# Optimization experiments

Measured on AMD Instinct MI355X. Metric: run time of the kernel, lower is better.

The kernel has to match this reference:

```python
import jax, jax.numpy as jnp
import numpy as np
from jax import lax

L, B, S, D, V, NL = 64, 32, 64, 512, 32000, 2


def setup_inputs() -> dict:
    key = jax.random.key(0)
    ks = jax.random.split(key, 9)
    sd = 1.0 / np.sqrt(D)
    return {
        "rnn_input": jax.random.randint(ks[0], (L, B), 0, V),
        "last_hidden": jax.random.normal(ks[1], (NL, B, D), jnp.float32),
        "encoder_outputs": jax.random.normal(ks[2], (S, B, D), jnp.float32),
        "embed_table": jax.random.normal(ks[3], (V, D), jnp.float32) * sd,
        "sru_W": jax.random.normal(ks[4], (NL, D, 3 * D), jnp.float32) * sd,
        "sru_b": jax.random.normal(ks[5], (NL, 2 * D), jnp.float32) * 0.01,
        "attn_W": jax.random.normal(ks[6], (2 * D, D), jnp.float32) * sd,
        "out_W": jax.random.normal(ks[7], (D, V), jnp.float32) * sd,
        "out_b": jax.random.normal(ks[8], (V,), jnp.float32) * 0.01,
    }


def _sru_layer(x, c0, W, b):
    # x: [L,B,D] layer input, c0: [B,D], W: [D,3D], b: [2D]
    U = jnp.einsum('lbd,de->lbe', x, W)          # [L,B,3D]
    z, fp, rp = jnp.split(U, 3, axis=-1)          # candidate, forget, reset pre-acts
    bf, br = jnp.split(b, 2)
    f = jax.nn.sigmoid(fp + bf)
    r = jax.nn.sigmoid(rp + br)

    def step(c, inp):
        f_t, z_t = inp
        c = f_t * c + (1.0 - f_t) * z_t
        return c, c

    c_last, c_seq = lax.scan(step, c0, (f, z))    # c_seq: [L,B,D]
    h = r * jnp.tanh(c_seq) + (1.0 - r) * x       # highway (n_in == n_out)
    return h, c_last


def reference(rnn_input, last_hidden, encoder_outputs, embed_table, sru_W, sru_b, attn_W, out_W, out_b):
    x = embed_table[rnn_input]                    # [L,B,D]
    finals = []
    for l in range(NL):                           # small fixed layer loop
        x, c_last = _sru_layer(x, last_hidden[l], sru_W[l], sru_b[l])
        finals.append(c_last)
    hidden = jnp.stack(finals, axis=0)            # [NL,B,D]

    q = jnp.transpose(x, (1, 0, 2))               # [B,L,D]
    mem = jnp.transpose(encoder_outputs, (1, 0, 2))  # [B,S,D]
    scores = jnp.einsum('bld,bsd->bls', q, mem)   # dot attention
    align = jax.nn.softmax(scores, axis=-1)
    ctx = jnp.einsum('bls,bsd->bld', align, mem)
    attn_h = jnp.tanh(jnp.concatenate([ctx, q], axis=-1) @ attn_W)  # [B,L,D]
    output = attn_h @ out_W + out_b               # [B,L,V]
    return output, hidden
```

## Files before the change

kernel.cpp:

```cpp
#include <hip/hip_runtime.h>
#include <hip/hip_bf16.h>

#define L_ 64
#define B_ 32
#define S_ 64
#define D_ 512
#define V_ 32000
#define NL_ 2

typedef __attribute__((ext_vector_type(8))) short bf16x8;
typedef __attribute__((ext_vector_type(4))) float f32x4;

static __device__ __forceinline__ short f2bf(float f) {
  union { float f; unsigned u; } x; x.f = f;
  unsigned r = (x.u + 0x7FFFu + ((x.u >> 16) & 1u)) >> 16;
  return (short)r;
}

#define GLOAD_LDS16(g, l)                                                     \
  __builtin_amdgcn_global_load_lds(                                           \
      (const __attribute__((address_space(1))) void*)(g),                     \
      (__attribute__((address_space(3))) void*)(l), 16, 0, 0)

__global__ void prep_kernel(const float* __restrict__ sruW, const float* __restrict__ attnW,
                            const float* __restrict__ outW, const int* __restrict__ tok,
                            const float* __restrict__ tab,
                            short* __restrict__ WTs, short* __restrict__ WTa,
                            short* __restrict__ WTo,
                            float* __restrict__ xf, short* __restrict__ xb) {
  int bid = blockIdx.x;
  int tx = threadIdx.x, ty = threadIdx.y;
  __shared__ float tile[32][33];
  if (bid < 18048) {
    const float* in;
    short* out;
    int K, N, bx, by;
    if (bid < 1536) {
      int l = (bid >= 768) ? 1 : 0;
      int r = bid - l * 768;
      bx = r % 48; by = r / 48; K = 512; N = 1536;
      in = sruW + (size_t)l * 512 * 1536;
      out = WTs + (size_t)l * 1536 * 512;
    } else if (bid < 2048) {
      int r = bid - 1536;
      bx = r % 16; by = r / 16; K = 1024; N = 512;
      in = attnW; out = WTa;
    } else {
      int r = bid - 2048;
      bx = r % 1000; by = r / 1000; K = 512; N = 32000;
      in = outW; out = WTo;
    }
    int x = bx * 32 + tx;
    int y0 = by * 32;
    for (int j = ty; j < 32; j += 8) {
      int y = y0 + j;
      tile[j][tx] = (x < N && y < K) ? in[(size_t)y * N + x] : 0.f;
    }
    __syncthreads();
    int xo = y0 + tx;
    int yo0 = bx * 32;
    for (int j = ty; j < 32; j += 8) {
      int yo = yo0 + j;
      if (yo < N && xo < K) out[(size_t)yo * K + xo] = f2bf(tile[tx][j]);
    }
  } else {
    int i = (bid - 18048) * 256 + ty * 32 + tx;
    int d = i & (D_ - 1);
    int lb = i >> 9;
    float v = tab[(size_t)tok[lb] * D_ + d];
    xf[i] = v;
    xb[i] = f2bf(v);
  }
}

template <int BMt, int BNt, int WM, int WN, int MODE>
__global__ __launch_bounds__(256) void gemm_t(
    const short* __restrict__ A, const short* __restrict__ BT,
    void* __restrict__ Cptr, const float* __restrict__ bias,
    int M, int N, int K, int nbm) {
  constexpr int MI = BMt / WM / 16;
  constexpr int NI = BNt / WN / 16;
  constexpr int ACH = BMt / 8;
  constexpr int NCH = (BMt + BNt) / 8;
  constexpr int CPW = NCH / 4;

  const int nwg = gridDim.x;
  const int qc = nwg >> 3;
  const int bid = blockIdx.x;
  const int wg = (bid & 7) * qc + (bid >> 3);
  const int bm = wg % nbm;
  const int bn = wg / nbm;

  __shared__ __align__(16) short la[2][BMt * 64];
  __shared__ __align__(16) short lb[2][BNt * 64];
  const int tid = threadIdx.x;
  const int wave = tid >> 6, lane = tid & 63;
  const int wm = (wave / WN) * (BMt / WM);
  const int wn = (wave % WN) * (BNt / WN);

  f32x4 acc[MI][NI] = {};

  const int lrow = lane >> 3;
  const int lslot = lane & 7;
  const short* Abase = A + (size_t)(bm * BMt) * K;
  const short* Bbase = BT + (size_t)(bn * BNt) * K;

  auto stage = [&](int buf, int k0) {
#pragma unroll
    for (int c = 0; c < CPW; ++c) {
      int chunk = wave * CPW + c;
      if (chunk < ACH) {
        int row = chunk * 8 + lrow;
        int slot = lslot ^ (row & 7);
        GLOAD_LDS16(Abase + (size_t)row * K + k0 + slot * 8, &la[buf][chunk * 512]);
      } else {
        int bc = chunk - ACH;
        int row = bc * 8 + lrow;
        int slot = lslot ^ (row & 7);
        GLOAD_LDS16(Bbase + (size_t)row * K + k0 + slot * 8, &lb[buf][bc * 512]);
      }
    }
  };

  stage(0, 0);
  __syncthreads();

  const int nt = K / 64;
  int cur = 0;
  for (int t = 0; t < nt; ++t) {
    if (t + 1 < nt) stage(cur ^ 1, (t + 1) * 64);
#pragma unroll
    for (int kk = 0; kk < 2; ++kk) {
      bf16x8 af[MI], bfr[NI];
#pragma unroll
      for (int mi = 0; mi < MI; ++mi) {
        int row = wm + mi * 16 + (lane & 15);
        int slot = (kk * 4 + (lane >> 4)) ^ (row & 7);
        af[mi] = *(const bf16x8*)&la[cur][row * 64 + slot * 8];
      }
#pragma unroll
      for (int ni = 0; ni < NI; ++ni) {
        int row = wn + ni * 16 + (lane & 15);
        int slot = (kk * 4 + (lane >> 4)) ^ (row & 7);
        bfr[ni] = *(const bf16x8*)&lb[cur][row * 64 + slot * 8];
      }
#pragma unroll
      for (int mi = 0; mi < MI; ++mi)
#pragma unroll
        for (int ni = 0; ni < NI; ++ni)
          acc[mi][ni] = __builtin_amdgcn_mfma_f32_16x16x32_bf16(
              af[mi], bfr[ni], acc[mi][ni], 0, 0, 0);
    }
    __syncthreads();
    cur ^= 1;
  }

  const int cl = lane & 15;
  const int rl = (lane >> 4) * 4;
#pragma unroll
  for (int mi = 0; mi < MI; ++mi) {
#pragma unroll
    for (int ni = 0; ni < NI; ++ni) {
      int c = bn * BNt + wn + ni * 16 + cl;
      int r0 = bm * BMt + wm + mi * 16 + rl;
#pragma unroll
      for (int j = 0; j < 4; ++j) {
        int r = r0 + j;
        float v = acc[mi][ni][j];
        if (MODE == 0) {
          ((float*)Cptr)[(size_t)r * N + c] = v;
        } else if (MODE == 1) {
          ((short*)Cptr)[(size_t)r * N + c] = f2bf(tanhf(v));
        } else {
          int b = r & 31, l = r >> 5;
          ((float*)Cptr)[(size_t)(b * L_ + l) * N + c] = v + bias[c];
        }
      }
    }
  }
}

template <int MODE>
__global__ __launch_bounds__(256, 3) void gemm_s(
    const short* __restrict__ A, const short* __restrict__ BT,
    void* __restrict__ Cptr, const float* __restrict__ bias,
    int M, int N, int K, int nbm) {
  const int nwg = gridDim.x;
  const int qc = nwg >> 3;
  const int bid = blockIdx.x;
  const int wg = (bid & 7) * qc + (bid >> 3);
  const int bm = wg % nbm;
  const int bn = wg / nbm;

  __shared__ __align__(16) short la[128 * 64];
  __shared__ __align__(16) short lb[128 * 64];
  const int tid = threadIdx.x;
  const int wave = tid >> 6, lane = tid & 63;
  const int wm = (wave >> 1) * 64, wn = (wave & 1) * 64;

  f32x4 acc[4][4] = {};

  const int lrow = lane >> 3;
  const int lslot = lane & 7;
  const short* Abase = A + (size_t)(bm * 128) * K;
  const short* Bbase = BT + (size_t)(bn * 128) * K;

  const int nt = K / 64;
  for (int t = 0; t < nt; ++t) {
    const int k0 = t * 64;
#pragma unroll
    for (int c = 0; c < 4; ++c) {
      int chunk = wave * 4 + c;
      int row = chunk * 8 + lrow;
      int slot = lslot ^ (row & 7);
      GLOAD_LDS16(Abase + (size_t)row * K + k0 + slot * 8, &la[chunk * 512]);
      GLOAD_LDS16(Bbase + (size_t)row * K + k0 + slot * 8, &lb[chunk * 512]);
    }
    __syncthreads();
#pragma unroll
    for (int kk = 0; kk < 2; ++kk) {
      bf16x8 af[4], bfr[4];
#pragma unroll
      for (int mi = 0; mi < 4; ++mi) {
        int row = wm + mi * 16 + (lane & 15);
        int slot = (kk * 4 + (lane >> 4)) ^ (row & 7);
        af[mi] = *(const bf16x8*)&la[row * 64 + slot * 8];
      }
#pragma unroll
      for (int ni = 0; ni < 4; ++ni) {
        int row = wn + ni * 16 + (lane & 15);
        int slot = (kk * 4 + (lane >> 4)) ^ (row & 7);
        bfr[ni] = *(const bf16x8*)&lb[row * 64 + slot * 8];
      }
#pragma unroll
      for (int mi = 0; mi < 4; ++mi)
#pragma unroll
        for (int ni = 0; ni < 4; ++ni)
          acc[mi][ni] = __builtin_amdgcn_mfma_f32_16x16x32_bf16(
              af[mi], bfr[ni], acc[mi][ni], 0, 0, 0);
    }
    __syncthreads();
  }

  const int cl = lane & 15;
  const int rl = (lane >> 4) * 4;
#pragma unroll
  for (int mi = 0; mi < 4; ++mi) {
#pragma unroll
    for (int ni = 0; ni < 4; ++ni) {
      int c = bn * 128 + wn + ni * 16 + cl;
      int r0 = bm * 128 + wm + mi * 16 + rl;
      float bs = (MODE == 2) ? bias[c] : 0.f;
#pragma unroll
      for (int j = 0; j < 4; ++j) {
        int r = r0 + j;
        float v = acc[mi][ni][j];
        if (MODE == 2) {
          int b = r & 31, l = r >> 5;
          ((float*)Cptr)[(size_t)(b * L_ + l) * N + c] = v + bs;
        } else {
          ((float*)Cptr)[(size_t)r * N + c] = v;
        }
      }
    }
  }
}

__global__ void sru_scan_kernel(const float* __restrict__ U, const float* __restrict__ bvec,
                                const float* __restrict__ xin, const float* __restrict__ c0,
                                float* __restrict__ hf, short* __restrict__ hb,
                                float* __restrict__ clast) {
  int idx = blockIdx.x * 64 + threadIdx.x;
  int b = idx >> 9, d = idx & 511;
  float c = c0[idx];
  const float bfb = bvec[d], brb = bvec[512 + d];
  const float* Ub = U + (size_t)b * 1536 + d;
  const float* Xb = xin + (size_t)b * 512 + d;

  for (int l0 = 0; l0 < L_; l0 += 8) {
    float z[8], fp[8], rp[8], xv[8];
#pragma unroll
    for (int j = 0; j < 8; ++j) {
      size_t u = (size_t)(l0 + j) * B_ * 1536;
      z[j] = Ub[u];
      fp[j] = Ub[u + 512];
      rp[j] = Ub[u + 1024];
      xv[j] = Xb[(size_t)(l0 + j) * B_ * 512];
    }
#pragma unroll
    for (int j = 0; j < 8; ++j) {
      float f = 1.f / (1.f + expf(-(fp[j] + bfb)));
      float r = 1.f / (1.f + expf(-(rp[j] + brb)));
      c = f * c + (1.f - f) * z[j];
      float h = r * tanhf(c) + (1.f - r) * xv[j];
      size_t o = ((size_t)(l0 + j) * B_ + b) * 512 + d;
      hf[o] = h;
      hb[o] = f2bf(h);
    }
  }
  clast[idx] = c;
}

__global__ __launch_bounds__(256) void attn_fused_kernel(
    const float* __restrict__ x, const float* __restrict__ enc,
    const short* __restrict__ xq, short* __restrict__ cat) {
  __shared__ float q[512];
  __shared__ float al[64];
  int r = blockIdx.x;
  int b = r & (B_ - 1);
  int tid = threadIdx.x;
  int wave = tid >> 6, lane = tid & 63;
  for (int d = tid; d < 512; d += 256) {
    q[d] = x[(size_t)r * 512 + d];
    cat[(size_t)r * 1024 + 512 + d] = xq[(size_t)r * 512 + d];
  }
  __syncthreads();
#pragma unroll
  for (int si = 0; si < 16; ++si) {
    int s = wave * 16 + si;
    const float* m = enc + ((size_t)s * B_ + b) * 512;
    float a = 0.f;
#pragma unroll
    for (int k = 0; k < 8; ++k) a += q[lane + k * 64] * m[lane + k * 64];
    for (int o = 32; o > 0; o >>= 1) a += __shfl_xor(a, o);
    if (lane == 0) al[s] = a;
  }
  __syncthreads();
  if (tid < 64) {
    float v = al[tid];
    float mx = v;
    for (int o = 32; o > 0; o >>= 1) mx = fmaxf(mx, __shfl_xor(mx, o));
    float e = expf(v - mx);
    float sm = e;
    for (int o = 32; o > 0; o >>= 1) sm += __shfl_xor(sm, o);
    al[tid] = e / sm;
  }
  __syncthreads();
  for (int d = tid; d < 512; d += 256) {
    float acc = 0.f;
#pragma unroll 16
    for (int s = 0; s < S_; ++s) acc += al[s] * enc[((size_t)s * B_ + b) * 512 + d];
    cat[(size_t)r * 1024 + d] = f2bf(acc);
  }
}

extern "C" void kernel_launch(void* const* d_in, const int* in_sizes, int n_in,
                              void* d_out, int out_size, void* d_ws, size_t ws_size,
                              hipStream_t stream) {
  const int* rnn = (const int*)d_in[0];
  const float* h0 = (const float*)d_in[1];
  const float* enc = (const float*)d_in[2];
  const float* tab = (const float*)d_in[3];
  const float* sruW = (const float*)d_in[4];
  const float* srub = (const float*)d_in[5];
  const float* attnW = (const float*)d_in[6];
  const float* outW = (const float*)d_in[7];
  const float* outb = (const float*)d_in[8];
  float* out = (float*)d_out;

  char* ws = (char*)d_ws;
  size_t off = 0;
  auto alloc = [&](size_t bytes) {
    char* p = ws + off;
    off += (bytes + 255) & ~(size_t)255;
    return p;
  };
  float* xf = (float*)alloc(4ull * 2048 * 512);
  float* xf2 = (float*)alloc(4ull * 2048 * 512);
  short* xb = (short*)alloc(2ull * 2048 * 512);
  float* U = (float*)alloc(4ull * 2048 * 1536);
  short* WTs = (short*)alloc(2ull * 2 * 1536 * 512);
  short* WTa = (short*)alloc(2ull * 512 * 1024);
  short* WTo = (short*)alloc(2ull * 32000 * 512);
  short* cat = (short*)alloc(2ull * 2048 * 1024);
  short* ah = (short*)alloc(2ull * 2048 * 512);

  prep_kernel<<<22144, dim3(32, 8), 0, stream>>>(sruW, attnW, outW, rnn, tab,
                                                 WTs, WTa, WTo, xf, xb);

  float* hidden_out = out + (size_t)B_ * L_ * V_;

  gemm_t<64, 128, 1, 4, 0><<<384, 256, 0, stream>>>(xb, WTs, U, nullptr, 2048, 1536, 512, 32);
  sru_scan_kernel<<<256, 64, 0, stream>>>(U, srub, xf, h0, xf2, xb, hidden_out);
  gemm_t<64, 128, 1, 4, 0><<<384, 256, 0, stream>>>(xb, WTs + 1536 * 512, U, nullptr,
                                                    2048, 1536, 512, 32);
  sru_scan_kernel<<<256, 64, 0, stream>>>(U, srub + 1024, xf2, h0 + B_ * D_, xf, xb,
                                          hidden_out + B_ * D_);

  attn_fused_kernel<<<2048, 256, 0, stream>>>(xf, enc, xb, cat);

  gemm_t<64, 64, 2, 2, 1><<<256, 256, 0, stream>>>(cat, WTa, ah, nullptr, 2048, 512, 1024, 32);
  gemm_s<2><<<4000, 256, 0, stream>>>(ah, WTo, out, outb, 2048, 32000, 512, 16);
}
```

Before: 231.7 us.

## Fuse SRU sigmoid gates into GEMM epilogue and batch attention over 8 queries

```diff
diff --git a/kernel.cpp b/kernel.cpp
--- a/kernel.cpp
+++ b/kernel.cpp
@@ -171,9 +171,9 @@
           ((float*)Cptr)[(size_t)r * N + c] = v;
         } else if (MODE == 1) {
           ((short*)Cptr)[(size_t)r * N + c] = f2bf(tanhf(v));
-        } else {
-          int b = r & 31, l = r >> 5;
-          ((float*)Cptr)[(size_t)(b * L_ + l) * N + c] = v + bias[c];
+        } else if (MODE == 3) {
+          if (c >= 512) v = 1.f / (1.f + expf(-(v + bias[c - 512])));
+          ((float*)Cptr)[(size_t)r * N + c] = v;
         }
       }
     }
@@ -181,7 +181,7 @@
 }
 
 template <int MODE>
-__global__ __launch_bounds__(256, 3) void gemm_s(
+__global__ __launch_bounds__(256, 4) void gemm_s(
     const short* __restrict__ A, const short* __restrict__ BT,
     void* __restrict__ Cptr, const float* __restrict__ bias,
     int M, int N, int K, int nbm) {
@@ -266,33 +266,30 @@
   }
 }
 
-__global__ void sru_scan_kernel(const float* __restrict__ U, const float* __restrict__ bvec,
+__global__ void sru_scan_kernel(const float* __restrict__ U,
                                 const float* __restrict__ xin, const float* __restrict__ c0,
                                 float* __restrict__ hf, short* __restrict__ hb,
                                 float* __restrict__ clast) {
   int idx = blockIdx.x * 64 + threadIdx.x;
   int b = idx >> 9, d = idx & 511;
   float c = c0[idx];
-  const float bfb = bvec[d], brb = bvec[512 + d];
   const float* Ub = U + (size_t)b * 1536 + d;
   const float* Xb = xin + (size_t)b * 512 + d;
 
   for (int l0 = 0; l0 < L_; l0 += 8) {
-    float z[8], fp[8], rp[8], xv[8];
+    float z[8], f[8], r[8], xv[8];
 #pragma unroll
     for (int j = 0; j < 8; ++j) {
       size_t u = (size_t)(l0 + j) * B_ * 1536;
       z[j] = Ub[u];
-      fp[j] = Ub[u + 512];
-      rp[j] = Ub[u + 1024];
+      f[j] = Ub[u + 512];
+      r[j] = Ub[u + 1024];
       xv[j] = Xb[(size_t)(l0 + j) * B_ * 512];
     }
 #pragma unroll
     for (int j = 0; j < 8; ++j) {
-      float f = 1.f / (1.f + expf(-(fp[j] + bfb)));
-      float r = 1.f / (1.f + expf(-(rp[j] + brb)));
-      c = f * c + (1.f - f) * z[j];
-      float h = r * tanhf(c) + (1.f - r) * xv[j];
+      c = f[j] * c + (1.f - f[j]) * z[j];
+      float h = r[j] * tanhf(c) + (1.f - r[j]) * xv[j];
       size_t o = ((size_t)(l0 + j) * B_ + b) * 512 + d;
       hf[o] = h;
       hb[o] = f2bf(h);
@@ -301,46 +298,65 @@
   clast[idx] = c;
 }
 
-__global__ __launch_bounds__(256) void attn_fused_kernel(
+__global__ __launch_bounds__(256) void attn_fused2_kernel(
     const float* __restrict__ x, const float* __restrict__ enc,
     const short* __restrict__ xq, short* __restrict__ cat) {
-  __shared__ float q[512];
-  __shared__ float al[64];
-  int r = blockIdx.x;
-  int b = r & (B_ - 1);
+  __shared__ float q[8][512];
+  __shared__ float sc[8][64];
+  __shared__ float al[8][64];
+  int bid = blockIdx.x;
+  int b = bid & 31, lo = bid >> 5;
   int tid = threadIdx.x;
   int wave = tid >> 6, lane = tid & 63;
-  for (int d = tid; d < 512; d += 256) {
-    q[d] = x[(size_t)r * 512 + d];
-    cat[(size_t)r * 1024 + 512 + d] = xq[(size_t)r * 512 + d];
+
+  for (int i = tid; i < 8 * 512; i += 256) {
+    int li = i >> 9, d = i & 511;
+    size_t r = (size_t)((lo * 8 + li) * B_ + b);
+    q[li][d] = x[r * 512 + d];
+    cat[r * 1024 + 512 + d] = xq[r * 512 + d];
   }
   __syncthreads();
-#pragma unroll
+
   for (int si = 0; si < 16; ++si) {
     int s = wave * 16 + si;
     const float* m = enc + ((size_t)s * B_ + b) * 512;
-    float a = 0.f;
-#pragma unroll
-    for (int k = 0; k < 8; ++k) a += q[lane + k * 64] * m[lane + k * 64];
-    for (int o = 32; o > 0; o >>= 1) a += __shfl_xor(a, o);
-    if (lane == 0) al[s] = a;
+    float ev[8];
+#pragma unroll
+    for (int k = 0; k < 8; ++k) ev[k] = m[lane + 64 * k];
+#pragma unroll
+    for (int li = 0; li < 8; ++li) {
+      float a = 0.f;
+#pragma unroll
+      for (int k = 0; k < 8; ++k) a += ev[k] * q[li][lane + 64 * k];
+      for (int o = 32; o > 0; o >>= 1) a += __shfl_xor(a, o);
+      if (lane == 0) sc[li][s] = a;
+    }
   }
   __syncthreads();
-  if (tid < 64) {
-    float v = al[tid];
+
+#pragma unroll
+  for (int rr = 0; rr < 2; ++rr) {
+    int li = wave * 2 + rr;
+    float v = sc[li][lane];
     float mx = v;
     for (int o = 32; o > 0; o >>= 1) mx = fmaxf(mx, __shfl_xor(mx, o));
     float e = expf(v - mx);
     float sm = e;
     for (int o = 32; o > 0; o >>= 1) sm += __shfl_xor(sm, o);
-    al[tid] = e / sm;
+    al[li][lane] = e / sm;
   }
   __syncthreads();
+
   for (int d = tid; d < 512; d += 256) {
-    float acc = 0.f;
-#pragma unroll 16
-    for (int s = 0; s < S_; ++s) acc += al[s] * enc[((size_t)s * B_ + b) * 512 + d];
-    cat[(size_t)r * 1024 + d] = f2bf(acc);
+    float acc[8] = {};
+    for (int s = 0; s < S_; ++s) {
+      float e = enc[((size_t)s * B_ + b) * 512 + d];
+#pragma unroll
+      for (int li = 0; li < 8; ++li) acc[li] += al[li][s] * e;
+    }
+#pragma unroll
+    for (int li = 0; li < 8; ++li)
+      cat[((size_t)((lo * 8 + li) * B_ + b)) * 1024 + d] = f2bf(acc[li]);
   }
 }
 
@@ -380,14 +396,14 @@
 
   float* hidden_out = out + (size_t)B_ * L_ * V_;
 
-  gemm_t<64, 128, 1, 4, 0><<<384, 256, 0, stream>>>(xb, WTs, U, nullptr, 2048, 1536, 512, 32);
-  sru_scan_kernel<<<256, 64, 0, stream>>>(U, srub, xf, h0, xf2, xb, hidden_out);
-  gemm_t<64, 128, 1, 4, 0><<<384, 256, 0, stream>>>(xb, WTs + 1536 * 512, U, nullptr,
+  gemm_t<64, 128, 1, 4, 3><<<384, 256, 0, stream>>>(xb, WTs, U, srub, 2048, 1536, 512, 32);
+  sru_scan_kernel<<<256, 64, 0, stream>>>(U, xf, h0, xf2, xb, hidden_out);
+  gemm_t<64, 128, 1, 4, 3><<<384, 256, 0, stream>>>(xb, WTs + 1536 * 512, U, srub + 1024,
                                                     2048, 1536, 512, 32);
-  sru_scan_kernel<<<256, 64, 0, stream>>>(U, srub + 1024, xf2, h0 + B_ * D_, xf, xb,
+  sru_scan_kernel<<<256, 64, 0, stream>>>(U, xf2, h0 + B_ * D_, xf, xb,
                                           hidden_out + B_ * D_);
 
-  attn_fused_kernel<<<2048, 256, 0, stream>>>(xf, enc, xb, cat);
+  attn_fused2_kernel<<<256, 256, 0, stream>>>(xf, enc, xb, cat);
 
   gemm_t<64, 64, 2, 2, 1><<<256, 256, 0, stream>>>(cat, WTa, ah, nullptr, 2048, 512, 1024, 32);
   gemm_s<2><<<4000, 256, 0, stream>>>(ah, WTo, out, outb, 2048, 32000, 512, 16);
```

Result: slower. 250.9 us (+8.3%).
